# Kernel tuning notes

Measured on AMD Instinct MI355X. Metric: run time of the kernel, lower is better.

The kernel has to match this reference:

```python
import jax, jax.numpy as jnp
import numpy as np
import math

B, S, D, H = 2, 2048, 1024, 16
HD = D // H  # 64


def _rope(x, cos, sin):
    # x: [B,S,H,HD]; cos/sin: [S, HD//2]
    x2 = x.reshape(*x.shape[:-1], HD // 2, 2)
    x0, x1 = x2[..., 0], x2[..., 1]
    c = cos[None, :, None, :]
    s = sin[None, :, None, :]
    r0 = x0 * c - x1 * s
    r1 = x0 * s + x1 * c
    return jnp.stack([r0, r1], axis=-1).reshape(x.shape)


def setup_inputs() -> dict:
    key = jax.random.key(0)
    ks = jax.random.split(key, 6)
    x = jax.random.normal(ks[0], (B, S, D), dtype=jnp.float32)
    wq = jax.random.normal(ks[1], (D, D), dtype=jnp.float32) * 0.02
    wk = jax.random.normal(ks[2], (D, D), dtype=jnp.float32) * 0.02
    wv = jax.random.normal(ks[3], (D, D), dtype=jnp.float32) * 0.02
    wo = jax.random.normal(ks[4], (D, D), dtype=jnp.float32) * 0.02
    # standard RoPE frequencies: theta = 10000^(-2i/HD)
    inv_freq = 1.0 / (10000.0 ** (jnp.arange(0, HD, 2, dtype=jnp.float32) / HD))
    t = jnp.arange(S, dtype=jnp.float32)
    ang = t[:, None] * inv_freq[None, :]  # [S, HD//2]
    freqs_cos = jnp.cos(ang)
    freqs_sin = jnp.sin(ang)
    # causal additive mask [S, S]
    mask = jnp.where(jnp.tril(jnp.ones((S, S), dtype=bool)), 0.0, -1e9).astype(jnp.float32)
    return {"x": x, "wq": wq, "wk": wk, "wv": wv, "wo": wo,
            "freqs_cos": freqs_cos, "freqs_sin": freqs_sin, "mask": mask}


def reference(x, wq, wk, wv, wo, freqs_cos, freqs_sin, mask):
    b, s, d = x.shape
    # nn.Linear with no bias: y = x @ W^T
    q = jnp.einsum('bsd,od->bso', x, wq).reshape(b, s, H, HD)
    k = jnp.einsum('bsd,od->bso', x, wk).reshape(b, s, H, HD)
    v = jnp.einsum('bsd,od->bso', x, wv).reshape(b, s, H, HD)
    q = _rope(q, freqs_cos, freqs_sin)
    k = _rope(k, freqs_cos, freqs_sin)
    # [B,H,S,HD]
    q = q.transpose(0, 2, 1, 3)
    k = k.transpose(0, 2, 1, 3)
    v = v.transpose(0, 2, 1, 3)
    scores = jnp.einsum('bhqd,bhkd->bhqk', q, k) / math.sqrt(HD)
    scores = scores + mask[None, None, :, :]
    p = jax.nn.softmax(scores.astype(jnp.float32), axis=-1).astype(q.dtype)
    out = jnp.einsum('bhqk,bhkd->bhqd', p, v)
    out = out.transpose(0, 2, 1, 3).reshape(b, s, d)
    return jnp.einsum('bsd,od->bso', out, wo)
```

## Files before the change

kernel.cpp:

```cpp
#include <hip/hip_runtime.h>
#include <hip/hip_bf16.h>
#include <stdint.h>

#define NB 2
#define NS 2048
#define ND 1024
#define NH 16
#define NM (NB*NS)

typedef __attribute__((ext_vector_type(8))) short bf16x8;
typedef __attribute__((ext_vector_type(4))) float f32x4;

static __device__ __forceinline__ f32x4 mfma16(bf16x8 a, bf16x8 b, f32x4 c) {
  return __builtin_amdgcn_mfma_f32_16x16x32_bf16(a, b, c, 0, 0, 0);
}

static __device__ __forceinline__ void gload_lds16(const void* g, void* l) {
  __builtin_amdgcn_global_load_lds(
      (const __attribute__((address_space(1))) void*)g,
      (__attribute__((address_space(3))) void*)l, 16, 0, 0);
}

static __device__ __forceinline__ uint32_t pkbf2(float a, float b) {
  return (uint32_t)__bfloat16_as_ushort(__float2bfloat16(a)) |
         ((uint32_t)__bfloat16_as_ushort(__float2bfloat16(b)) << 16);
}

#define QSCALE 0.18033688011112042f

struct alignas(8) bh4 { __hip_bfloat16 x, y, z, w; };

__global__ void cvt_all(const float* __restrict__ x,
                        const float* __restrict__ w0, const float* __restrict__ w1,
                        const float* __restrict__ w2, const float* __restrict__ w3,
                        __hip_bfloat16* xb, __hip_bfloat16* o0, __hip_bfloat16* o1,
                        __hip_bfloat16* o2, __hip_bfloat16* o3) {
  const int b = blockIdx.x;
  const float* in;
  __hip_bfloat16* out;
  int i;
  if (b < 4096) { in = x; out = xb; i = b * 256 + threadIdx.x; }
  else {
    const int t = (b - 4096) >> 10;
    in  = (t == 0) ? w0 : (t == 1) ? w1 : (t == 2) ? w2 : w3;
    out = (t == 0) ? o0 : (t == 1) ? o1 : (t == 2) ? o2 : o3;
    i = ((b - 4096) & 1023) * 256 + threadIdx.x;
  }
  float4 v = reinterpret_cast<const float4*>(in)[i];
  bh4 o;
  o.x = __float2bfloat16(v.x);
  o.y = __float2bfloat16(v.y);
  o.z = __float2bfloat16(v.z);
  o.w = __float2bfloat16(v.w);
  reinterpret_cast<bh4*>(out)[i] = o;
}

__global__ __launch_bounds__(256) void gemm_qkv(
    const __hip_bfloat16* __restrict__ A,
    const __hip_bfloat16* __restrict__ Wq,
    const __hip_bfloat16* __restrict__ Wk,
    const __hip_bfloat16* __restrict__ Wv,
    const float* __restrict__ fcos,
    const float* __restrict__ fsin,
    __hip_bfloat16* __restrict__ Qo,
    __hip_bfloat16* __restrict__ Ko,
    __hip_bfloat16* __restrict__ Vo) {
  __shared__ __hip_bfloat16 sA[128 * 32];
  __shared__ __hip_bfloat16 sB[128 * 32];
  __shared__ __align__(16) char xtr[33792];

  const int bl = blockIdx.x;
  const int logical = (bl & 7) * 96 + (bl >> 3);
  const int xt = logical / 24;
  const int yy = logical - xt * 24;
  const int wsel = yy >> 3;
  const __hip_bfloat16* W = (wsel == 0) ? Wq : (wsel == 1) ? Wk : Wv;

  const int tid = threadIdx.x;
  const int wid = tid >> 6;
  const int lane = tid & 63;
  const int l4 = lane >> 4, l16 = lane & 15;
  const int brow = xt * 128;
  const int bcol = (yy & 7) * 128;
  const int wr = (wid >> 1) * 64;
  const int wc = (wid & 1) * 64;
  const int ss0 = brow & 2047;
  const int bbb = brow >> 11;

  if (wsel < 2) {
    float2* tab = (float2*)xtr;
#pragma unroll
    for (int i = 0; i < 4; ++i) {
      const int e = i * 1024 + tid * 4;
      const int ssl = e >> 5, p = e & 31;
      float4 c4 = *(const float4*)&fcos[(ss0 + ssl) * 32 + p];
      float4 s4 = *(const float4*)&fsin[(ss0 + ssl) * 32 + p];
      tab[ssl * 33 + p + 0] = {c4.x, s4.x};
      tab[ssl * 33 + p + 1] = {c4.y, s4.y};
      tab[ssl * 33 + p + 2] = {c4.z, s4.z};
      tab[ssl * 33 + p + 3] = {c4.w, s4.w};
    }
  }

  f32x4 acc[4][4] = {};

  const __hip_bfloat16* Ap = A + (size_t)(brow + (tid >> 2)) * 1024 + (tid & 3) * 8;
  const __hip_bfloat16* Wp = W + (size_t)(bcol + (tid >> 2)) * 1024 + (tid & 3) * 8;
  char* sAc = (char*)sA + wid * 1024;
  char* sBc = (char*)sB + wid * 1024;

  for (int kt = 0; kt < 32; ++kt) {
    const int k0 = kt * 32;
    __syncthreads();
    gload_lds16(Ap + k0,             sAc);
    gload_lds16(Ap + 64 * 1024 + k0, sAc + 4096);
    gload_lds16(Wp + k0,             sBc);
    gload_lds16(Wp + 64 * 1024 + k0, sBc + 4096);
    __syncthreads();

    bf16x8 af[4], bfr[4];
#pragma unroll
    for (int i = 0; i < 4; ++i)
      af[i] = *(const bf16x8*)&sA[(wr + i * 16 + l16) * 32 + l4 * 8];
#pragma unroll
    for (int i = 0; i < 4; ++i)
      bfr[i] = *(const bf16x8*)&sB[(wc + i * 16 + l16) * 32 + l4 * 8];
#pragma unroll
    for (int mi = 0; mi < 4; ++mi)
#pragma unroll
      for (int ni = 0; ni < 4; ++ni)
        acc[mi][ni] = mfma16(af[mi], bfr[ni], acc[mi][ni]);
  }

  if (wsel == 2) {
    __hip_bfloat16 (*tt)[132] = (__hip_bfloat16(*)[132])xtr;
#pragma unroll
    for (int h = 0; h < 2; ++h) {
      __syncthreads();
      if ((wid & 1) == h) {
#pragma unroll
        for (int mi = 0; mi < 4; ++mi)
#pragma unroll
          for (int ni = 0; ni < 4; ++ni) {
            const int c = ni * 16 + l16;
            const int r0 = wr + mi * 16 + l4 * 4;
            uint2 w;
            w.x = pkbf2(acc[mi][ni][0], acc[mi][ni][1]);
            w.y = pkbf2(acc[mi][ni][2], acc[mi][ni][3]);
            *(uint2*)&tt[c][r0] = w;
          }
      }
      __syncthreads();
      const int cl = tid >> 2;
      const int rq = (tid & 3) * 32;
      const int o = bcol + h * 64 + cl;
      const int hh = o >> 6, hd = o & 63;
      __hip_bfloat16* dst =
          Vo + ((size_t)(bbb * 16 + hh) * 64 + hd) * 2048 + ss0 + rq;
#pragma unroll
      for (int k2 = 0; k2 < 4; ++k2)
        *(uint4*)&dst[k2 * 8] = *(const uint4*)&tt[cl][rq + k2 * 8];
    }
  } else {
    const float2* tab = (const float2*)xtr;
    __hip_bfloat16* dst = (wsel == 0) ? Qo : Ko;
#pragma unroll
    for (int mi = 0; mi < 4; ++mi)
#pragma unroll
      for (int ni = 0; ni < 4; ++ni)
#pragma unroll
        for (int j = 0; j < 4; ++j) {
          float v = acc[mi][ni][j];
          const int rloc = wr + mi * 16 + l4 * 4 + j;
          const int col = bcol + wc + ni * 16 + l16;
          const int hh = col >> 6, hd = col & 63;
          float other = __shfl_xor(v, 1);
          const float2 cs = tab[rloc * 33 + (hd >> 1)];
          float r = (col & 1) ? (other * cs.y + v * cs.x)
                              : (v * cs.x - other * cs.y);
          if (wsel == 0) r *= QSCALE;
          dst[((size_t)(bbb * 16 + hh) * 2048 + ss0 + rloc) * 64 + hd] =
              __float2bfloat16(r);
        }
  }
}

__global__ __launch_bounds__(256) void gemm_out(
    const __hip_bfloat16* __restrict__ A,
    const __hip_bfloat16* __restrict__ W,
    float* __restrict__ C) {
  __shared__ __hip_bfloat16 sA[64 * 32];
  __shared__ __hip_bfloat16 sB[128 * 32];

  const int bl = blockIdx.x;
  const int logical = (bl & 7) * 64 + (bl >> 3);
  const int tid = threadIdx.x;
  const int wid = tid >> 6;
  const int lane = tid & 63;
  const int l4 = lane >> 4, l16 = lane & 15;
  const int brow = (logical >> 3) * 64;
  const int bcol = (logical & 7) * 128;
  const int wr = (wid & 1) * 32;
  const int wc = (wid >> 1) * 64;

  f32x4 acc[2][4] = {};

  const __hip_bfloat16* Ap = A + (size_t)(brow + (tid >> 2)) * 1024 + (tid & 3) * 8;
  const __hip_bfloat16* Wp = W + (size_t)(bcol + (tid >> 2)) * 1024 + (tid & 3) * 8;
  char* sAc = (char*)sA + wid * 1024;
  char* sBc = (char*)sB + wid * 1024;

  for (int kt = 0; kt < 32; ++kt) {
    const int k0 = kt * 32;
    __syncthreads();
    gload_lds16(Ap + k0,             sAc);
    gload_lds16(Wp + k0,             sBc);
    gload_lds16(Wp + 64 * 1024 + k0, sBc + 4096);
    __syncthreads();

    bf16x8 af[2], bfr[4];
#pragma unroll
    for (int i = 0; i < 2; ++i)
      af[i] = *(const bf16x8*)&sA[(wr + i * 16 + l16) * 32 + l4 * 8];
#pragma unroll
    for (int i = 0; i < 4; ++i)
      bfr[i] = *(const bf16x8*)&sB[(wc + i * 16 + l16) * 32 + l4 * 8];
#pragma unroll
    for (int mi = 0; mi < 2; ++mi)
#pragma unroll
      for (int ni = 0; ni < 4; ++ni)
        acc[mi][ni] = mfma16(af[mi], bfr[ni], acc[mi][ni]);
  }

#pragma unroll
  for (int mi = 0; mi < 2; ++mi)
#pragma unroll
    for (int ni = 0; ni < 4; ++ni)
#pragma unroll
      for (int j = 0; j < 4; ++j) {
        const int row = brow + wr + mi * 16 + l4 * 4 + j;
        const int col = bcol + wc + ni * 16 + l16;
        C[(size_t)row * 1024 + col] = acc[mi][ni][j];
      }
}

__global__ __launch_bounds__(256) void attn_fwd(
    const __hip_bfloat16* __restrict__ Q,
    const __hip_bfloat16* __restrict__ K,
    const __hip_bfloat16* __restrict__ VT,
    __hip_bfloat16* __restrict__ AO) {
  const int L = blockIdx.x;
  int qt, bh;
  if (L < 256) { qt = 15 - (L >> 5); bh = L & 31; }
  else         { qt = (L >> 5) - 8;  bh = L & 31; }
  const int bb = bh >> 4;
  const int hh = bh & 15;
  const int tid = threadIdx.x;
  const int wid = tid >> 6;
  const int lane = tid & 63;
  const int l4 = lane >> 4, l16 = lane & 15;
  const int wq0 = qt * 128 + wid * 32;

  const __hip_bfloat16* Qg = Q + (size_t)bh * 2048 * 64;
  const __hip_bfloat16* Kg = K + (size_t)bh * 2048 * 64;
  const __hip_bfloat16* Vg = VT + (size_t)bh * 64 * 2048;

  __shared__ __align__(16) char sKb[2][8192];
  __shared__ __align__(16) char sVb[2][8192];
  __shared__ __hip_bfloat16 sP[4][32][72];

  bf16x8 qf[2][2];
#pragma unroll
  for (int q2 = 0; q2 < 2; ++q2)
#pragma unroll
    for (int dk = 0; dk < 2; ++dk)
      qf[q2][dk] = *(const bf16x8*)&Qg[(size_t)(wq0 + q2 * 16 + l16) * 64 + dk * 32 + l4 * 8];

  const int srow = lane >> 3;
  const int scol = ((lane & 7) ^ srow) * 8;
  const int fo0 = l16 * 128 + (((l4) ^ (l16 & 7)) * 16);
  const int fo1 = l16 * 128 + (((4 + l4) ^ (l16 & 7)) * 16);

  float lrun[2] = {0.f, 0.f};
  f32x4 oacc[2][4] = {};

  const int nkv = 2 * qt + 2;

#pragma unroll
  for (int i = 0; i < 2; ++i) {
    const int c = wid * 2 + i;
    gload_lds16(Kg + (size_t)(c * 8 + srow) * 64 + scol,   &sKb[0][c * 1024]);
    gload_lds16(Vg + (size_t)(c * 8 + srow) * 2048 + scol, &sVb[0][c * 1024]);
  }

  for (int kv = 0; kv < nkv; ++kv) {
    const int cur = kv & 1;
    const int kb = kv * 64;
    __syncthreads();

    if (kv + 1 < nkv) {
      const int kb2 = kb + 64;
#pragma unroll
      for (int i = 0; i < 2; ++i) {
        const int c = wid * 2 + i;
        gload_lds16(Kg + (size_t)(kb2 + c * 8 + srow) * 64 + scol,   &sKb[cur ^ 1][c * 1024]);
        gload_lds16(Vg + (size_t)(c * 8 + srow) * 2048 + kb2 + scol, &sVb[cur ^ 1][c * 1024]);
      }
    }

    if (kb <= wq0 + 31) {
      bf16x8 kfr[4][2];
#pragma unroll
      for (int kf = 0; kf < 4; ++kf) {
        kfr[kf][0] = *(const bf16x8*)&sKb[cur][kf * 2048 + fo0];
        kfr[kf][1] = *(const bf16x8*)&sKb[cur][kf * 2048 + fo1];
      }

      f32x4 sacc[4][2] = {};
      __builtin_amdgcn_s_setprio(1);
#pragma unroll
      for (int dk = 0; dk < 2; ++dk)
#pragma unroll
        for (int kf = 0; kf < 4; ++kf)
#pragma unroll
          for (int q2 = 0; q2 < 2; ++q2)
            sacc[kf][q2] = mfma16(kfr[kf][dk], qf[q2][dk], sacc[kf][q2]);
      __builtin_amdgcn_s_setprio(0);

      bf16x8 vfr[4][2];
#pragma unroll
      for (int df = 0; df < 4; ++df) {
        vfr[df][0] = *(const bf16x8*)&sVb[cur][df * 2048 + fo0];
        vfr[df][1] = *(const bf16x8*)&sVb[cur][df * 2048 + fo1];
      }

      const bool need_mask = (kb + 63 > wq0);
#pragma unroll
      for (int q2 = 0; q2 < 2; ++q2) {
        const int qi = wq0 + q2 * 16 + l16;
        float pe[16];
#pragma unroll
        for (int kf = 0; kf < 4; ++kf)
#pragma unroll
          for (int j = 0; j < 4; ++j) {
            float s = sacc[kf][q2][j];
            if (need_mask && (kb + kf * 16 + l4 * 4 + j > qi)) s = -1e30f;
            pe[kf * 4 + j] = exp2f(s);
          }
#pragma unroll
        for (int kf = 0; kf < 4; ++kf) {
          uint2 w;
          w.x = pkbf2(pe[kf * 4 + 0], pe[kf * 4 + 1]);
          w.y = pkbf2(pe[kf * 4 + 2], pe[kf * 4 + 3]);
          *(uint2*)&sP[wid][q2 * 16 + l16][kf * 16 + l4 * 4] = w;
        }
        float ts = 0.f;
#pragma unroll
        for (int t = 0; t < 16; ++t) ts += pe[t];
        ts += __shfl_xor(ts, 16);
        ts += __shfl_xor(ts, 32);
        lrun[q2] += ts;
      }

      __builtin_amdgcn_s_setprio(1);
#pragma unroll
      for (int ks = 0; ks < 2; ++ks) {
        bf16x8 pfr[2];
#pragma unroll
        for (int mf = 0; mf < 2; ++mf)
          pfr[mf] = *(const bf16x8*)&sP[wid][mf * 16 + l16][ks * 32 + l4 * 8];
#pragma unroll
        for (int mf = 0; mf < 2; ++mf)
#pragma unroll
          for (int df = 0; df < 4; ++df)
            oacc[mf][df] = mfma16(pfr[mf], vfr[df][ks], oacc[mf][df]);
      }
      __builtin_amdgcn_s_setprio(0);
    }
  }

  float inv[2];
#pragma unroll
  for (int q2 = 0; q2 < 2; ++q2) inv[q2] = 1.f / lrun[q2];
#pragma unroll
  for (int mf = 0; mf < 2; ++mf)
#pragma unroll
    for (int j = 0; j < 4; ++j) {
      const float ir = __shfl(inv[mf], l4 * 4 + j);
      const int ss = wq0 + mf * 16 + l4 * 4 + j;
#pragma unroll
      for (int df = 0; df < 4; ++df) {
        const int dd = hh * 64 + df * 16 + l16;
        AO[((size_t)bb * 2048 + ss) * 1024 + dd] =
            __float2bfloat16(oacc[mf][df][j] * ir);
      }
    }
}

extern "C" void kernel_launch(void* const* d_in, const int* in_sizes, int n_in,
                              void* d_out, int out_size, void* d_ws, size_t ws_size,
                              hipStream_t stream) {
  const float* x  = (const float*)d_in[0];
  const float* wq = (const float*)d_in[1];
  const float* wk = (const float*)d_in[2];
  const float* wv = (const float*)d_in[3];
  const float* wo = (const float*)d_in[4];
  const float* fc = (const float*)d_in[5];
  const float* fs = (const float*)d_in[6];

  char* ws = (char*)d_ws;
  const size_t MB = 1024 * 1024;
  __hip_bfloat16* xb  = (__hip_bfloat16*)(ws);
  __hip_bfloat16* wqb = (__hip_bfloat16*)(ws + 8 * MB);
  __hip_bfloat16* wkb = (__hip_bfloat16*)(ws + 10 * MB);
  __hip_bfloat16* wvb = (__hip_bfloat16*)(ws + 12 * MB);
  __hip_bfloat16* wob = (__hip_bfloat16*)(ws + 14 * MB);
  __hip_bfloat16* qws = (__hip_bfloat16*)(ws + 16 * MB);
  __hip_bfloat16* kws = (__hip_bfloat16*)(ws + 24 * MB);
  __hip_bfloat16* vws = (__hip_bfloat16*)(ws + 32 * MB);
  __hip_bfloat16* ao  = (__hip_bfloat16*)(ws + 40 * MB);

  cvt_all<<<8192, 256, 0, stream>>>(x, wq, wk, wv, wo, xb, wqb, wkb, wvb, wob);

  gemm_qkv<<<768, 256, 0, stream>>>(xb, wqb, wkb, wvb, fc, fs, qws, kws, vws);

  attn_fwd<<<dim3(512), 256, 0, stream>>>(qws, kws, vws, ao);

  gemm_out<<<512, 256, 0, stream>>>(ao, wob, (float*)d_out);
}
```

Measured before the change: 227.7 us.

## Double-buffer LDS tiles in QKV and output GEMMs with one barrier per step

Both projection GEMMs now prefetch the next K-tile into a second LDS buffer while computing on the current one, cutting the barriers per iteration from two to one. The rope table fill is moved after the main loop so one LDS buffer can be shared by the tiles, the table and the transpose scratch. s_setprio raises wave priority around the MFMA block. Correctness depends on the compiler emitting waits for the async global-to-LDS loads before the barrier, and the rope table load now sits after the loop where it adds latency.

```diff
diff --git a/kernel.cpp b/kernel.cpp
--- a/kernel.cpp
+++ b/kernel.cpp
@@ -65,9 +65,7 @@
     __hip_bfloat16* __restrict__ Qo,
     __hip_bfloat16* __restrict__ Ko,
     __hip_bfloat16* __restrict__ Vo) {
-  __shared__ __hip_bfloat16 sA[128 * 32];
-  __shared__ __hip_bfloat16 sB[128 * 32];
-  __shared__ __align__(16) char xtr[33792];
+  __shared__ __align__(16) char smem[33792];
 
   const int bl = blockIdx.x;
   const int logical = (bl & 7) * 96 + (bl >> 3);
@@ -87,8 +85,81 @@
   const int ss0 = brow & 2047;
   const int bbb = brow >> 11;
 
-  if (wsel < 2) {
-    float2* tab = (float2*)xtr;
+  f32x4 acc[4][4] = {};
+
+  const __hip_bfloat16* Ap = A + (size_t)(brow + (tid >> 2)) * 1024 + (tid & 3) * 8;
+  const __hip_bfloat16* Wp = W + (size_t)(bcol + (tid >> 2)) * 1024 + (tid & 3) * 8;
+  const int wof = wid * 1024;
+
+  gload_lds16(Ap,             smem + wof);
+  gload_lds16(Ap + 64 * 1024, smem + wof + 4096);
+  gload_lds16(Wp,             smem + 8192 + wof);
+  gload_lds16(Wp + 64 * 1024, smem + 8192 + wof + 4096);
+  __syncthreads();
+
+  for (int kt = 0; kt < 32; ++kt) {
+    const int cur = kt & 1;
+    const char* sAb = smem + cur * 16384;
+    const char* sBb = smem + cur * 16384 + 8192;
+
+    if (kt + 1 < 32) {
+      const int k0 = (kt + 1) * 32;
+      char* sAn = smem + (cur ^ 1) * 16384 + wof;
+      char* sBn = smem + (cur ^ 1) * 16384 + 8192 + wof;
+      gload_lds16(Ap + k0,             sAn);
+      gload_lds16(Ap + 64 * 1024 + k0, sAn + 4096);
+      gload_lds16(Wp + k0,             sBn);
+      gload_lds16(Wp + 64 * 1024 + k0, sBn + 4096);
+    }
+
+    bf16x8 af[4], bfr[4];
+#pragma unroll
+    for (int i = 0; i < 4; ++i)
+      af[i] = *(const bf16x8*)(sAb + ((wr + i * 16 + l16) * 32 + l4 * 8) * 2);
+#pragma unroll
+    for (int i = 0; i < 4; ++i)
+      bfr[i] = *(const bf16x8*)(sBb + ((wc + i * 16 + l16) * 32 + l4 * 8) * 2);
+    __builtin_amdgcn_s_setprio(1);
+#pragma unroll
+    for (int mi = 0; mi < 4; ++mi)
+#pragma unroll
+      for (int ni = 0; ni < 4; ++ni)
+        acc[mi][ni] = mfma16(af[mi], bfr[ni], acc[mi][ni]);
+    __builtin_amdgcn_s_setprio(0);
+    __syncthreads();
+  }
+
+  if (wsel == 2) {
+    __hip_bfloat16 (*tt)[132] = (__hip_bfloat16(*)[132])smem;
+#pragma unroll
+    for (int h = 0; h < 2; ++h) {
+      __syncthreads();
+      if ((wid & 1) == h) {
+#pragma unroll
+        for (int mi = 0; mi < 4; ++mi)
+#pragma unroll
+          for (int ni = 0; ni < 4; ++ni) {
+            const int c = ni * 16 + l16;
+            const int r0 = wr + mi * 16 + l4 * 4;
+            uint2 w;
+            w.x = pkbf2(acc[mi][ni][0], acc[mi][ni][1]);
+            w.y = pkbf2(acc[mi][ni][2], acc[mi][ni][3]);
+            *(uint2*)&tt[c][r0] = w;
+          }
+      }
+      __syncthreads();
+      const int cl = tid >> 2;
+      const int rq = (tid & 3) * 32;
+      const int o = bcol + h * 64 + cl;
+      const int hh = o >> 6, hd = o & 63;
+      __hip_bfloat16* dst =
+          Vo + ((size_t)(bbb * 16 + hh) * 64 + hd) * 2048 + ss0 + rq;
+#pragma unroll
+      for (int k2 = 0; k2 < 4; ++k2)
+        *(uint4*)&dst[k2 * 8] = *(const uint4*)&tt[cl][rq + k2 * 8];
+    }
+  } else {
+    float2* tab = (float2*)smem;
 #pragma unroll
     for (int i = 0; i < 4; ++i) {
       const int e = i * 1024 + tid * 4;
@@ -100,69 +171,7 @@
       tab[ssl * 33 + p + 2] = {c4.z, s4.z};
       tab[ssl * 33 + p + 3] = {c4.w, s4.w};
     }
-  }
-
-  f32x4 acc[4][4] = {};
-
-  const __hip_bfloat16* Ap = A + (size_t)(brow + (tid >> 2)) * 1024 + (tid & 3) * 8;
-  const __hip_bfloat16* Wp = W + (size_t)(bcol + (tid >> 2)) * 1024 + (tid & 3) * 8;
-  char* sAc = (char*)sA + wid * 1024;
-  char* sBc = (char*)sB + wid * 1024;
-
-  for (int kt = 0; kt < 32; ++kt) {
-    const int k0 = kt * 32;
     __syncthreads();
-    gload_lds16(Ap + k0,             sAc);
-    gload_lds16(Ap + 64 * 1024 + k0, sAc + 4096);
-    gload_lds16(Wp + k0,             sBc);
-    gload_lds16(Wp + 64 * 1024 + k0, sBc + 4096);
-    __syncthreads();
-
-    bf16x8 af[4], bfr[4];
-#pragma unroll
-    for (int i = 0; i < 4; ++i)
-      af[i] = *(const bf16x8*)&sA[(wr + i * 16 + l16) * 32 + l4 * 8];
-#pragma unroll
-    for (int i = 0; i < 4; ++i)
-      bfr[i] = *(const bf16x8*)&sB[(wc + i * 16 + l16) * 32 + l4 * 8];
-#pragma unroll
-    for (int mi = 0; mi < 4; ++mi)
-#pragma unroll
-      for (int ni = 0; ni < 4; ++ni)
-        acc[mi][ni] = mfma16(af[mi], bfr[ni], acc[mi][ni]);
-  }
-
-  if (wsel == 2) {
-    __hip_bfloat16 (*tt)[132] = (__hip_bfloat16(*)[132])xtr;
-#pragma unroll
-    for (int h = 0; h < 2; ++h) {
-      __syncthreads();
-      if ((wid & 1) == h) {
-#pragma unroll
-        for (int mi = 0; mi < 4; ++mi)
-#pragma unroll
-          for (int ni = 0; ni < 4; ++ni) {
-            const int c = ni * 16 + l16;
-            const int r0 = wr + mi * 16 + l4 * 4;
-            uint2 w;
-            w.x = pkbf2(acc[mi][ni][0], acc[mi][ni][1]);
-            w.y = pkbf2(acc[mi][ni][2], acc[mi][ni][3]);
-            *(uint2*)&tt[c][r0] = w;
-          }
-      }
-      __syncthreads();
-      const int cl = tid >> 2;
-      const int rq = (tid & 3) * 32;
-      const int o = bcol + h * 64 + cl;
-      const int hh = o >> 6, hd = o & 63;
-      __hip_bfloat16* dst =
-          Vo + ((size_t)(bbb * 16 + hh) * 64 + hd) * 2048 + ss0 + rq;
-#pragma unroll
-      for (int k2 = 0; k2 < 4; ++k2)
-        *(uint4*)&dst[k2 * 8] = *(const uint4*)&tt[cl][rq + k2 * 8];
-    }
-  } else {
-    const float2* tab = (const float2*)xtr;
     __hip_bfloat16* dst = (wsel == 0) ? Qo : Ko;
 #pragma unroll
     for (int mi = 0; mi < 4; ++mi)
@@ -189,8 +198,7 @@
     const __hip_bfloat16* __restrict__ A,
     const __hip_bfloat16* __restrict__ W,
     float* __restrict__ C) {
-  __shared__ __hip_bfloat16 sA[64 * 32];
-  __shared__ __hip_bfloat16 sB[128 * 32];
+  __shared__ __align__(16) char smem[24576];
 
   const int bl = blockIdx.x;
   const int logical = (bl & 7) * 64 + (bl >> 3);
@@ -207,29 +215,42 @@
 
   const __hip_bfloat16* Ap = A + (size_t)(brow + (tid >> 2)) * 1024 + (tid & 3) * 8;
   const __hip_bfloat16* Wp = W + (size_t)(bcol + (tid >> 2)) * 1024 + (tid & 3) * 8;
-  char* sAc = (char*)sA + wid * 1024;
-  char* sBc = (char*)sB + wid * 1024;
+  const int wof = wid * 1024;
+
+  gload_lds16(Ap,             smem + wof);
+  gload_lds16(Wp,             smem + 4096 + wof);
+  gload_lds16(Wp + 64 * 1024, smem + 4096 + wof + 4096);
+  __syncthreads();
 
   for (int kt = 0; kt < 32; ++kt) {
-    const int k0 = kt * 32;
-    __syncthreads();
-    gload_lds16(Ap + k0,             sAc);
-    gload_lds16(Wp + k0,             sBc);
-    gload_lds16(Wp + 64 * 1024 + k0, sBc + 4096);
-    __syncthreads();
+    const int cur = kt & 1;
+    const char* sAb = smem + cur * 12288;
+    const char* sBb = smem + cur * 12288 + 4096;
+
+    if (kt + 1 < 32) {
+      const int k0 = (kt + 1) * 32;
+      char* sAn = smem + (cur ^ 1) * 12288 + wof;
+      char* sBn = smem + (cur ^ 1) * 12288 + 4096 + wof;
+      gload_lds16(Ap + k0,             sAn);
+      gload_lds16(Wp + k0,             sBn);
+      gload_lds16(Wp + 64 * 1024 + k0, sBn + 4096);
+    }
 
     bf16x8 af[2], bfr[4];
 #pragma unroll
     for (int i = 0; i < 2; ++i)
-      af[i] = *(const bf16x8*)&sA[(wr + i * 16 + l16) * 32 + l4 * 8];
+      af[i] = *(const bf16x8*)(sAb + ((wr + i * 16 + l16) * 32 + l4 * 8) * 2);
 #pragma unroll
     for (int i = 0; i < 4; ++i)
-      bfr[i] = *(const bf16x8*)&sB[(wc + i * 16 + l16) * 32 + l4 * 8];
+      bfr[i] = *(const bf16x8*)(sBb + ((wc + i * 16 + l16) * 32 + l4 * 8) * 2);
+    __builtin_amdgcn_s_setprio(1);
 #pragma unroll
     for (int mi = 0; mi < 2; ++mi)
 #pragma unroll
       for (int ni = 0; ni < 4; ++ni)
         acc[mi][ni] = mfma16(af[mi], bfr[ni], acc[mi][ni]);
+    __builtin_amdgcn_s_setprio(0);
+    __syncthreads();
   }
 
 #pragma unroll
```

After: 223.6 us. No clear change (-1.8%).
